# Performance work log

Measured on AMD Instinct MI355X. Metric: run time of the kernel, lower is better.

The kernel has to match this reference:

```python
import jax, jax.numpy as jnp
import numpy as np

B, T, NW, NF = 4, 1, 1536, 16
N_CROSS = 400_000
N_EDGES = 1_600_000
C_OUT = 4
IN_DIM = 2 * NF + 2  # 34


def setup_inputs() -> dict:
    key = jax.random.key(0)
    ks = jax.random.split(key, 16)
    return {
        "first_wires": jax.random.normal(ks[0], (B, T, NW, NF), jnp.float32),
        "second_wires": jax.random.normal(ks[1], (B, T, NW, NF), jnp.float32),
        "crossings": jax.random.normal(ks[2], (N_CROSS, 2), jnp.float32),
        "bbox": jax.random.uniform(ks[3], (3,), jnp.float32) + 0.5,
        "edge_attr": jax.random.normal(ks[4], (N_EDGES, 4), jnp.float32),
        "indices": jax.random.randint(ks[5], (N_CROSS, 2), 0, NW),
        "edge_index": jax.random.randint(ks[6], (2, N_EDGES), 0, N_CROSS),
        "W": jax.random.normal(ks[7], (IN_DIM, C_OUT), jnp.float32) / np.sqrt(IN_DIM),
        "att_src": jax.random.normal(ks[8], (C_OUT,), jnp.float32),
        "att_dst": jax.random.normal(ks[9], (C_OUT,), jnp.float32),
        "W_e": jax.random.normal(ks[10], (4, C_OUT), jnp.float32) / 2.0,
        "att_edge": jax.random.normal(ks[11], (C_OUT,), jnp.float32),
        "bias": jnp.zeros((C_OUT,), jnp.float32),
        "w_mlp": jax.random.normal(ks[12], (C_OUT, 1), jnp.float32) / 2.0,
        "b_mlp": jnp.zeros((1,), jnp.float32),
    }


def reference(first_wires, second_wires, crossings, bbox, edge_attr,
              indices, edge_index, W, att_src, att_dst, W_e, att_edge,
              bias, w_mlp, b_mlp):
    b, t = first_wires.shape[0], first_wires.shape[1]
    n = indices.shape[0]
    # fill_window: gather wire features for each crossing and append normalized coords
    fw = first_wires[:, :, indices[:, 0], :]          # [B,T,N,NF]
    sw = second_wires[:, :, indices[:, 1], :]         # [B,T,N,NF]
    xc = crossings / jnp.linalg.norm(bbox)            # [N,2]
    xc = jnp.broadcast_to(xc[None, None], (b, t, n, 2))
    x = jnp.concatenate([fw, sw, xc], axis=-1)        # [B,T,N,2NF+2]
    x = x.reshape(b * t, n, -1)

    src, dst = edge_index[0], edge_index[1]
    h = x @ W                                          # [BT,N,C]
    a_e = (edge_attr @ W_e) @ att_edge                 # [E]

    def gat(hb):
        hs, hd = hb[src], hb[dst]                      # [E,C]
        logits = jax.nn.leaky_relu(hs @ att_src + hd @ att_dst + a_e, 0.2)
        m = jax.ops.segment_max(logits, dst, num_segments=n)
        ex = jnp.exp(logits - m[dst])
        den = jax.ops.segment_sum(ex, dst, num_segments=n)
        alpha = ex / (den[dst] + 1e-16)
        return jax.ops.segment_sum(alpha[:, None] * hs, dst, num_segments=n) + bias

    out = jax.vmap(gat)(h)                             # [BT,N,C]
    y = out @ w_mlp + b_mlp                            # [BT,N,1]
    return y.reshape(b, t, n, 1)
```

## Files before the change

kernel.cpp:

```cpp
#include <hip/hip_runtime.h>
#include <math.h>

#define BB 4
#define NWIRE 1536
#define NFEAT 16
#define BS 256
#define NBLK 256
#define DSHIFT 8
#define DPB (1 << DSHIFT)
#define MAXNB 2048

__global__ void k_wires(const float* __restrict__ fw, const float* __restrict__ sw,
                        const float* __restrict__ W, const float* __restrict__ att_src,
                        const float* __restrict__ att_dst, const float* __restrict__ wmlp,
                        float4* __restrict__ fwpre, float4* __restrict__ swpre) {
    int t = blockIdx.x * blockDim.x + threadIdx.x;
    if (t >= BB * NWIRE) return;
    const float* fp = fw + (size_t)t * NFEAT;
    const float* sp = sw + (size_t)t * NFEAT;
    float hf[4] = {0, 0, 0, 0}, hs[4] = {0, 0, 0, 0};
    #pragma unroll
    for (int k = 0; k < NFEAT; ++k) {
        float a = fp[k], b = sp[k];
        #pragma unroll
        for (int c = 0; c < 4; ++c) {
            hf[c] = fmaf(a, W[k * 4 + c], hf[c]);
            hs[c] = fmaf(b, W[(NFEAT + k) * 4 + c], hs[c]);
        }
    }
    float fs = 0, fd = 0, fq = 0, ss = 0, sd = 0, sq = 0;
    #pragma unroll
    for (int c = 0; c < 4; ++c) {
        float as = att_src[c], ad = att_dst[c], wm = wmlp[c];
        fs = fmaf(hf[c], as, fs); fd = fmaf(hf[c], ad, fd); fq = fmaf(hf[c], wm, fq);
        ss = fmaf(hs[c], as, ss); sd = fmaf(hs[c], ad, sd); sq = fmaf(hs[c], wm, sq);
    }
    fwpre[t] = make_float4(fs, fd, fq, 0.0f);
    swpre[t] = make_float4(ss, sd, sq, 0.0f);
}

__global__ void k_nodes(const int* __restrict__ indices, const float* __restrict__ crossings,
                        const float* __restrict__ bbox, const float* __restrict__ W,
                        const float* __restrict__ att_src, const float* __restrict__ att_dst,
                        const float* __restrict__ wmlp,
                        const float4* __restrict__ fwpre, const float4* __restrict__ swpre,
                        float2* __restrict__ srcb, float* __restrict__ dstb, int n) {
    int i = blockIdx.x * blockDim.x + threadIdx.x;
    if (i >= n) return;
    float inv = rsqrtf(bbox[0] * bbox[0] + bbox[1] * bbox[1] + bbox[2] * bbox[2]);
    int2 idx = ((const int2*)indices)[i];
    float2 xc = ((const float2*)crossings)[i];
    int i0 = idx.x, i1 = idx.y;
    float x0 = xc.x * inv, x1 = xc.y * inv;
    float xs = 0, xd = 0, xq = 0;
    #pragma unroll
    for (int c = 0; c < 4; ++c) {
        float hc = fmaf(x0, W[32 * 4 + c], x1 * W[33 * 4 + c]);
        xs = fmaf(hc, att_src[c], xs);
        xd = fmaf(hc, att_dst[c], xd);
        xq = fmaf(hc, wmlp[c], xq);
    }
    #pragma unroll
    for (int b = 0; b < BB; ++b) {
        float4 f = fwpre[b * NWIRE + i0];
        float4 s = swpre[b * NWIRE + i1];
        srcb[(size_t)b * n + i] = make_float2(f.x + s.x + xs, f.z + s.z + xq);
        dstb[(size_t)b * n + i] = f.y + s.y + xd;
    }
}

__global__ void k_binA1(const int* __restrict__ ei, int ne, int nb, int chunk,
                        int* __restrict__ bh) {
    __shared__ int lc[MAXNB];
    for (int i = threadIdx.x; i < nb; i += BS) lc[i] = 0;
    __syncthreads();
    int blk = blockIdx.x;
    const int* dstp = ei + ne;
    int e0 = blk * chunk, e1 = min(e0 + chunk, ne);
    int e = e0 + threadIdx.x * 4;
    for (; e + 3 < e1; e += BS * 4) {
        int4 d4 = *(const int4*)(dstp + e);
        atomicAdd(&lc[d4.x >> DSHIFT], 1);
        atomicAdd(&lc[d4.y >> DSHIFT], 1);
        atomicAdd(&lc[d4.z >> DSHIFT], 1);
        atomicAdd(&lc[d4.w >> DSHIFT], 1);
    }
    for (; e < e1; e += BS * 4) {
        int ke = min(e + 4, e1);
        for (int k = e; k < ke; ++k) atomicAdd(&lc[dstp[k] >> DSHIFT], 1);
    }
    __syncthreads();
    int* row = bh + (size_t)blk * nb;
    for (int b = threadIdx.x; b < nb; b += BS) row[b] = lc[b];
}

__global__ void k_scanBlk(int* __restrict__ bh, int* __restrict__ btot, int nb) {
    int b = blockIdx.x * blockDim.x + threadIdx.x;
    if (b >= nb) return;
    int run = 0;
    for (int k0 = 0; k0 < NBLK; k0 += 8) {
        int v[8];
        #pragma unroll
        for (int j = 0; j < 8; ++j) v[j] = bh[(size_t)(k0 + j) * nb + b];
        #pragma unroll
        for (int j = 0; j < 8; ++j) {
            int t = v[j];
            bh[(size_t)(k0 + j) * nb + b] = run;
            run += t;
        }
    }
    btot[b] = run;
}

__global__ void k_scanBuck(const int* __restrict__ btot, int* __restrict__ bbase,
                           int nb, int ne) {
    __shared__ int sh[1024];
    int t = threadIdx.x;
    int i0 = 2 * t, i1 = 2 * t + 1;
    int a = (i0 < nb) ? btot[i0] : 0;
    int b = (i1 < nb) ? btot[i1] : 0;
    sh[t] = a + b;
    __syncthreads();
    for (int ofs = 1; ofs < 1024; ofs <<= 1) {
        int u = (t >= ofs) ? sh[t - ofs] : 0;
        __syncthreads();
        sh[t] += u;
        __syncthreads();
    }
    int excl = sh[t] - (a + b);
    if (i0 < nb) bbase[i0] = excl;
    if (i1 < nb) bbase[i1] = excl + a;
    if (t == 0) bbase[nb] = ne;
}

__global__ void k_binA2(const int* __restrict__ ei, const float* __restrict__ eattr,
                        const float* __restrict__ We, const float* __restrict__ att_edge,
                        const int* __restrict__ bh, const int* __restrict__ bbase,
                        int ne, int nb, int chunk, int2* __restrict__ recs) {
    __shared__ int curs[MAXNB];
    int blk = blockIdx.x;
    const int* row = bh + (size_t)blk * nb;
    for (int b = threadIdx.x; b < nb; b += BS)
        curs[b] = bbase[b] + row[b];
    __syncthreads();
    float v0 = fmaf(We[0], att_edge[0], fmaf(We[1], att_edge[1], fmaf(We[2], att_edge[2], We[3] * att_edge[3])));
    float v1 = fmaf(We[4], att_edge[0], fmaf(We[5], att_edge[1], fmaf(We[6], att_edge[2], We[7] * att_edge[3])));
    float v2 = fmaf(We[8], att_edge[0], fmaf(We[9], att_edge[1], fmaf(We[10], att_edge[2], We[11] * att_edge[3])));
    float v3 = fmaf(We[12], att_edge[0], fmaf(We[13], att_edge[1], fmaf(We[14], att_edge[2], We[15] * att_edge[3])));
    const int* srcp = ei;
    const int* dstp = ei + ne;
    const float4* ea4 = (const float4*)eattr;
    int e0 = blk * chunk, e1 = min(e0 + chunk, ne);
    int e = e0 + threadIdx.x * 4;
    for (; e + 3 < e1; e += BS * 4) {
        int4 s4 = *(const int4*)(srcp + e);
        int4 d4 = *(const int4*)(dstp + e);
        float4 a0 = ea4[e], a1 = ea4[e + 1], a2 = ea4[e + 2], a3 = ea4[e + 3];
        float ae0 = fmaf(a0.x, v0, fmaf(a0.y, v1, fmaf(a0.z, v2, a0.w * v3)));
        float ae1 = fmaf(a1.x, v0, fmaf(a1.y, v1, fmaf(a1.z, v2, a1.w * v3)));
        float ae2 = fmaf(a2.x, v0, fmaf(a2.y, v1, fmaf(a2.z, v2, a2.w * v3)));
        float ae3 = fmaf(a3.x, v0, fmaf(a3.y, v1, fmaf(a3.z, v2, a3.w * v3)));
        int p0 = atomicAdd(&curs[d4.x >> DSHIFT], 1);
        int p1 = atomicAdd(&curs[d4.y >> DSHIFT], 1);
        int p2 = atomicAdd(&curs[d4.z >> DSHIFT], 1);
        int p3 = atomicAdd(&curs[d4.w >> DSHIFT], 1);
        recs[p0] = make_int2(((d4.x & (DPB - 1)) << 19) | s4.x, __float_as_int(ae0));
        recs[p1] = make_int2(((d4.y & (DPB - 1)) << 19) | s4.y, __float_as_int(ae1));
        recs[p2] = make_int2(((d4.z & (DPB - 1)) << 19) | s4.z, __float_as_int(ae2));
        recs[p3] = make_int2(((d4.w & (DPB - 1)) << 19) | s4.w, __float_as_int(ae3));
    }
    for (; e < e1; e += BS * 4) {
        int ke = min(e + 4, e1);
        for (int k = e; k < ke; ++k) {
            int s = srcp[k], d = dstp[k];
            float4 ea = ea4[k];
            float ae = fmaf(ea.x, v0, fmaf(ea.y, v1, fmaf(ea.z, v2, ea.w * v3)));
            int pos = atomicAdd(&curs[d >> DSHIFT], 1);
            recs[pos] = make_int2(((d & (DPB - 1)) << 19) | s, __float_as_int(ae));
        }
    }
}

__global__ void __launch_bounds__(BS)
k_gatB(const int2* __restrict__ recs, const int* __restrict__ bbase,
       const float2* __restrict__ srcb, const float* __restrict__ dstb,
       const float* __restrict__ bias, const float* __restrict__ wmlp,
       const float* __restrict__ bmlp, float* __restrict__ out, int n, int nb) {
    __shared__ float2 acc[DPB];
    __shared__ float pds[DPB];
    int g = blockIdx.x;
    int s = g & 7;
    int batch = s >> 1;
    int bucket = (g >> 3) * 2 + (s & 1);
    if (bucket >= nb) return;
    int r0 = bbase[bucket], r1 = bbase[bucket + 1];
    int dbase = bucket << DSHIFT;
    int dmax = min(DPB, n - dbase);
    const float* db = dstb + (size_t)batch * n;
    for (int i = threadIdx.x; i < DPB; i += BS) acc[i] = make_float2(0.0f, 0.0f);
    for (int i = threadIdx.x; i < dmax; i += BS) pds[i] = db[dbase + i];
    __syncthreads();
    const float2* sb = srcb + (size_t)batch * n;
    int i = r0 + threadIdx.x;
    for (; i + 3 * BS < r1; i += 4 * BS) {
        int2 ra = recs[i], rb = recs[i + BS], rc = recs[i + 2 * BS], rd = recs[i + 3 * BS];
        float2 pa = sb[ra.x & 0x7FFFF];
        float2 pb = sb[rb.x & 0x7FFFF];
        float2 pc = sb[rc.x & 0x7FFFF];
        float2 pd = sb[rd.x & 0x7FFFF];
        float lg, ex;
        int dlo;
        dlo = (unsigned)ra.x >> 19;
        lg = pa.x + pds[dlo] + __int_as_float(ra.y); lg = lg > 0.0f ? lg : 0.2f * lg; ex = expf(lg);
        atomicAdd(&acc[dlo].x, ex); atomicAdd(&acc[dlo].y, ex * pa.y);
        dlo = (unsigned)rb.x >> 19;
        lg = pb.x + pds[dlo] + __int_as_float(rb.y); lg = lg > 0.0f ? lg : 0.2f * lg; ex = expf(lg);
        atomicAdd(&acc[dlo].x, ex); atomicAdd(&acc[dlo].y, ex * pb.y);
        dlo = (unsigned)rc.x >> 19;
        lg = pc.x + pds[dlo] + __int_as_float(rc.y); lg = lg > 0.0f ? lg : 0.2f * lg; ex = expf(lg);
        atomicAdd(&acc[dlo].x, ex); atomicAdd(&acc[dlo].y, ex * pc.y);
        dlo = (unsigned)rd.x >> 19;
        lg = pd.x + pds[dlo] + __int_as_float(rd.y); lg = lg > 0.0f ? lg : 0.2f * lg; ex = expf(lg);
        atomicAdd(&acc[dlo].x, ex); atomicAdd(&acc[dlo].y, ex * pd.y);
    }
    for (; i < r1; i += BS) {
        int2 r = recs[i];
        float2 pq = sb[r.x & 0x7FFFF];
        int dlo = (unsigned)r.x >> 19;
        float lg = pq.x + pds[dlo] + __int_as_float(r.y);
        lg = lg > 0.0f ? lg : 0.2f * lg;
        float ex = expf(lg);
        atomicAdd(&acc[dlo].x, ex); atomicAdd(&acc[dlo].y, ex * pq.y);
    }
    __syncthreads();
    float cst = fmaf(bias[0], wmlp[0], fmaf(bias[1], wmlp[1], fmaf(bias[2], wmlp[2], bias[3] * wmlp[3]))) + bmlp[0];
    float* ob = out + (size_t)batch * n;
    for (int i2 = threadIdx.x; i2 < dmax; i2 += BS)
        ob[dbase + i2] = acc[i2].y / (acc[i2].x + 1e-16f) + cst;
}

extern "C" void kernel_launch(void* const* d_in, const int* in_sizes, int n_in,
                              void* d_out, int out_size, void* d_ws, size_t ws_size,
                              hipStream_t stream) {
    const float* first_wires  = (const float*)d_in[0];
    const float* second_wires = (const float*)d_in[1];
    const float* crossings    = (const float*)d_in[2];
    const float* bbox         = (const float*)d_in[3];
    const float* edge_attr    = (const float*)d_in[4];
    const int*   indices      = (const int*)d_in[5];
    const int*   edge_index   = (const int*)d_in[6];
    const float* W            = (const float*)d_in[7];
    const float* att_src      = (const float*)d_in[8];
    const float* att_dst      = (const float*)d_in[9];
    const float* W_e          = (const float*)d_in[10];
    const float* att_edge     = (const float*)d_in[11];
    const float* bias         = (const float*)d_in[12];
    const float* w_mlp        = (const float*)d_in[13];
    const float* b_mlp        = (const float*)d_in[14];
    float* out = (float*)d_out;

    const int n  = in_sizes[5] / 2;
    const int ne = in_sizes[6] / 2;
    const int nb = (n + DPB - 1) >> DSHIFT;
    const int nbp = (nb + 1) & ~1;
    const int chunk = (((ne + NBLK - 1) / NBLK) + 3) & ~3;

    char* ws = (char*)d_ws;
    size_t off = 0;
    float4* fwpre = (float4*)(ws + off); off += (size_t)BB * NWIRE * 16;
    float4* swpre = (float4*)(ws + off); off += (size_t)BB * NWIRE * 16;
    float2* srcb  = (float2*)(ws + off); off += (size_t)BB * n * 8;
    float*  dstb  = (float*)(ws + off);  off += (size_t)BB * n * 4;
    int*    bh    = (int*)(ws + off);    off += (size_t)nb * NBLK * 4;
    int*    btot  = (int*)(ws + off);    off += ((size_t)nb * 4 + 15) & ~15ull;
    int*    bbase = (int*)(ws + off);    off += ((size_t)(nb + 1) * 4 + 15) & ~15ull;
    int2*   recs  = (int2*)(ws + off);   off += (size_t)ne * 8;

    hipLaunchKernelGGL(k_wires, dim3((BB * NWIRE + BS - 1) / BS), dim3(BS), 0, stream,
                       first_wires, second_wires, W, att_src, att_dst, w_mlp, fwpre, swpre);
    hipLaunchKernelGGL(k_nodes, dim3((n + BS - 1) / BS), dim3(BS), 0, stream,
                       indices, crossings, bbox, W, att_src, att_dst, w_mlp,
                       fwpre, swpre, srcb, dstb, n);
    hipLaunchKernelGGL(k_binA1, dim3(NBLK), dim3(BS), 0, stream,
                       edge_index, ne, nb, chunk, bh);
    hipLaunchKernelGGL(k_scanBlk, dim3((nb + 63) / 64), dim3(64), 0, stream,
                       bh, btot, nb);
    hipLaunchKernelGGL(k_scanBuck, dim3(1), dim3(1024), 0, stream,
                       btot, bbase, nb, ne);
    hipLaunchKernelGGL(k_binA2, dim3(NBLK), dim3(BS), 0, stream,
                       edge_index, edge_attr, W_e, att_edge, bh, bbase, ne, nb, chunk, recs);
    hipLaunchKernelGGL(k_gatB, dim3(nbp * 4), dim3(BS), 0, stream,
                       recs, bbase, srcb, dstb, bias, w_mlp, b_mlp, out, n, nb);
}
```

Baseline: 249.1 us.

## Build per-destination CSR and replace shared-memory atomics with per-thread reductions

```diff
diff --git a/kernel.cpp b/kernel.cpp
--- a/kernel.cpp
+++ b/kernel.cpp
@@ -113,7 +113,7 @@
 }
 
 __global__ void k_scanBuck(const int* __restrict__ btot, int* __restrict__ bbase,
-                           int nb, int ne) {
+                           int* __restrict__ start, int nb, int n, int ne) {
     __shared__ int sh[1024];
     int t = threadIdx.x;
     int i0 = 2 * t, i1 = 2 * t + 1;
@@ -130,7 +130,7 @@
     int excl = sh[t] - (a + b);
     if (i0 < nb) bbase[i0] = excl;
     if (i1 < nb) bbase[i1] = excl + a;
-    if (t == 0) bbase[nb] = ne;
+    if (t == 0) { bbase[nb] = ne; start[n] = ne; }
 }
 
 __global__ void k_binA2(const int* __restrict__ ei, const float* __restrict__ eattr,
@@ -182,61 +182,83 @@
 }
 
 __global__ void __launch_bounds__(BS)
-k_gatB(const int2* __restrict__ recs, const int* __restrict__ bbase,
-       const float2* __restrict__ srcb, const float* __restrict__ dstb,
-       const float* __restrict__ bias, const float* __restrict__ wmlp,
-       const float* __restrict__ bmlp, float* __restrict__ out, int n, int nb) {
-    __shared__ float2 acc[DPB];
-    __shared__ float pds[DPB];
+k_binB(const int2* __restrict__ recs, const int* __restrict__ bbase,
+       int2* __restrict__ csr, int* __restrict__ start, int n, int nb) {
+    __shared__ int cnt[DPB];
+    __shared__ int tsum[BS];
+    int b = blockIdx.x;
+    int r0 = bbase[b], r1 = bbase[b + 1];
+    int nrec = r1 - r0;
+    cnt[threadIdx.x] = 0;
+    __syncthreads();
+    for (int i = threadIdx.x; i < nrec; i += BS)
+        atomicAdd(&cnt[(unsigned)recs[r0 + i].x >> 19], 1);
+    __syncthreads();
+    int c = cnt[threadIdx.x];
+    tsum[threadIdx.x] = c;
+    __syncthreads();
+    for (int ofs = 1; ofs < BS; ofs <<= 1) {
+        int u = (threadIdx.x >= ofs) ? tsum[threadIdx.x - ofs] : 0;
+        __syncthreads();
+        tsum[threadIdx.x] += u;
+        __syncthreads();
+    }
+    int excl = tsum[threadIdx.x] - c;
+    int d = (b << DSHIFT) + threadIdx.x;
+    if (d < n) start[d] = r0 + excl;
+    cnt[threadIdx.x] = excl;
+    __syncthreads();
+    for (int i = threadIdx.x; i < nrec; i += BS) {
+        int2 r = recs[r0 + i];
+        int dlo = (unsigned)r.x >> 19;
+        int pos = r0 + atomicAdd(&cnt[dlo], 1);
+        csr[pos] = make_int2(r.x & 0x7FFFF, r.y);
+    }
+}
+
+__global__ void __launch_bounds__(BS)
+k_gat(const int2* __restrict__ csr, const int* __restrict__ start,
+      const float2* __restrict__ srcb, const float* __restrict__ dstb,
+      const float* __restrict__ bias, const float* __restrict__ wmlp,
+      const float* __restrict__ bmlp, float* __restrict__ out, int n, int nb) {
     int g = blockIdx.x;
     int s = g & 7;
     int batch = s >> 1;
-    int bucket = (g >> 3) * 2 + (s & 1);
-    if (bucket >= nb) return;
-    int r0 = bbase[bucket], r1 = bbase[bucket + 1];
-    int dbase = bucket << DSHIFT;
-    int dmax = min(DPB, n - dbase);
-    const float* db = dstb + (size_t)batch * n;
-    for (int i = threadIdx.x; i < DPB; i += BS) acc[i] = make_float2(0.0f, 0.0f);
-    for (int i = threadIdx.x; i < dmax; i += BS) pds[i] = db[dbase + i];
-    __syncthreads();
+    int dblk = (g >> 3) * 2 + (s & 1);
+    if (dblk >= nb) return;
+    int d = (dblk << DSHIFT) + threadIdx.x;
+    if (d >= n) return;
+    int st = start[d], en = start[d + 1];
     const float2* sb = srcb + (size_t)batch * n;
-    int i = r0 + threadIdx.x;
-    for (; i + 3 * BS < r1; i += 4 * BS) {
-        int2 ra = recs[i], rb = recs[i + BS], rc = recs[i + 2 * BS], rd = recs[i + 3 * BS];
-        float2 pa = sb[ra.x & 0x7FFFF];
-        float2 pb = sb[rb.x & 0x7FFFF];
-        float2 pc = sb[rc.x & 0x7FFFF];
-        float2 pd = sb[rd.x & 0x7FFFF];
+    float pd = dstb[(size_t)batch * n + d];
+    float den = 0.0f, num = 0.0f;
+    int j = st;
+    for (; j + 4 <= en; j += 4) {
+        int2 r0 = csr[j], r1 = csr[j + 1], r2 = csr[j + 2], r3 = csr[j + 3];
+        float2 p0 = sb[r0.x];
+        float2 p1 = sb[r1.x];
+        float2 p2 = sb[r2.x];
+        float2 p3 = sb[r3.x];
         float lg, ex;
-        int dlo;
-        dlo = (unsigned)ra.x >> 19;
-        lg = pa.x + pds[dlo] + __int_as_float(ra.y); lg = lg > 0.0f ? lg : 0.2f * lg; ex = expf(lg);
-        atomicAdd(&acc[dlo].x, ex); atomicAdd(&acc[dlo].y, ex * pa.y);
-        dlo = (unsigned)rb.x >> 19;
-        lg = pb.x + pds[dlo] + __int_as_float(rb.y); lg = lg > 0.0f ? lg : 0.2f * lg; ex = expf(lg);
-        atomicAdd(&acc[dlo].x, ex); atomicAdd(&acc[dlo].y, ex * pb.y);
-        dlo = (unsigned)rc.x >> 19;
-        lg = pc.x + pds[dlo] + __int_as_float(rc.y); lg = lg > 0.0f ? lg : 0.2f * lg; ex = expf(lg);
-        atomicAdd(&acc[dlo].x, ex); atomicAdd(&acc[dlo].y, ex * pc.y);
-        dlo = (unsigned)rd.x >> 19;
-        lg = pd.x + pds[dlo] + __int_as_float(rd.y); lg = lg > 0.0f ? lg : 0.2f * lg; ex = expf(lg);
-        atomicAdd(&acc[dlo].x, ex); atomicAdd(&acc[dlo].y, ex * pd.y);
-    }
-    for (; i < r1; i += BS) {
-        int2 r = recs[i];
-        float2 pq = sb[r.x & 0x7FFFF];
-        int dlo = (unsigned)r.x >> 19;
-        float lg = pq.x + pds[dlo] + __int_as_float(r.y);
+        lg = p0.x + pd + __int_as_float(r0.y); lg = lg > 0.0f ? lg : 0.2f * lg;
+        ex = expf(lg); den += ex; num = fmaf(ex, p0.y, num);
+        lg = p1.x + pd + __int_as_float(r1.y); lg = lg > 0.0f ? lg : 0.2f * lg;
+        ex = expf(lg); den += ex; num = fmaf(ex, p1.y, num);
+        lg = p2.x + pd + __int_as_float(r2.y); lg = lg > 0.0f ? lg : 0.2f * lg;
+        ex = expf(lg); den += ex; num = fmaf(ex, p2.y, num);
+        lg = p3.x + pd + __int_as_float(r3.y); lg = lg > 0.0f ? lg : 0.2f * lg;
+        ex = expf(lg); den += ex; num = fmaf(ex, p3.y, num);
+    }
+    for (; j < en; ++j) {
+        int2 r = csr[j];
+        float2 pq = sb[r.x];
+        float lg = pq.x + pd + __int_as_float(r.y);
         lg = lg > 0.0f ? lg : 0.2f * lg;
         float ex = expf(lg);
-        atomicAdd(&acc[dlo].x, ex); atomicAdd(&acc[dlo].y, ex * pq.y);
-    }
-    __syncthreads();
+        den += ex; num = fmaf(ex, pq.y, num);
+    }
     float cst = fmaf(bias[0], wmlp[0], fmaf(bias[1], wmlp[1], fmaf(bias[2], wmlp[2], bias[3] * wmlp[3]))) + bmlp[0];
-    float* ob = out + (size_t)batch * n;
-    for (int i2 = threadIdx.x; i2 < dmax; i2 += BS)
-        ob[dbase + i2] = acc[i2].y / (acc[i2].x + 1e-16f) + cst;
+    out[(size_t)batch * n + d] = num / (den + 1e-16f) + cst;
 }
 
 extern "C" void kernel_launch(void* const* d_in, const int* in_sizes, int n_in,
@@ -274,7 +296,9 @@
     int*    bh    = (int*)(ws + off);    off += (size_t)nb * NBLK * 4;
     int*    btot  = (int*)(ws + off);    off += ((size_t)nb * 4 + 15) & ~15ull;
     int*    bbase = (int*)(ws + off);    off += ((size_t)(nb + 1) * 4 + 15) & ~15ull;
+    int*    start = (int*)(ws + off);    off += ((size_t)(n + 1) * 4 + 15) & ~15ull;
     int2*   recs  = (int2*)(ws + off);   off += (size_t)ne * 8;
+    int2*   csr   = (int2*)(ws + off);   off += (size_t)ne * 8;
 
     hipLaunchKernelGGL(k_wires, dim3((BB * NWIRE + BS - 1) / BS), dim3(BS), 0, stream,
                        first_wires, second_wires, W, att_src, att_dst, w_mlp, fwpre, swpre);
@@ -286,9 +310,11 @@
     hipLaunchKernelGGL(k_scanBlk, dim3((nb + 63) / 64), dim3(64), 0, stream,
                        bh, btot, nb);
     hipLaunchKernelGGL(k_scanBuck, dim3(1), dim3(1024), 0, stream,
-                       btot, bbase, nb, ne);
+                       btot, bbase, start, nb, n, ne);
     hipLaunchKernelGGL(k_binA2, dim3(NBLK), dim3(BS), 0, stream,
                        edge_index, edge_attr, W_e, att_edge, bh, bbase, ne, nb, chunk, recs);
-    hipLaunchKernelGGL(k_gatB, dim3(nbp * 4), dim3(BS), 0, stream,
-                       recs, bbase, srcb, dstb, bias, w_mlp, b_mlp, out, n, nb);
-}
+    hipLaunchKernelGGL(k_binB, dim3(nb), dim3(BS), 0, stream,
+                       recs, bbase, csr, start, n, nb);
+    hipLaunchKernelGGL(k_gat, dim3(nbp * 4), dim3(BS), 0, stream,
+                       csr, start, srcb, dstb, bias, w_mlp, b_mlp, out, n, nb);
+}
```

After: 234.5 us. -5.9%, faster.
